# Kernel tuning notes

Hardware: AMD Instinct MI355X
Metric: run time of the kernel (lower is better)

The kernel has to match this reference:

```python
import jax, jax.numpy as jnp
import numpy as np


def setup_inputs() -> dict:
    key = jax.random.key(0)
    ks = jax.random.split(key, 8)
    B, S, T, H, A = 4, 1024, 256, 512, 256
    return {
        "encoder_outputs": jax.random.normal(ks[0], (B, S, H), dtype=jnp.float32),
        "decoder_hidden": jax.random.normal(ks[1], (B, T, H), dtype=jnp.float32),
        "Wh": jax.random.normal(ks[2], (H, A), dtype=jnp.float32) * (1.0 / np.sqrt(H)),
        "bh": jax.random.normal(ks[3], (A,), dtype=jnp.float32) * 0.01,
        "Ws": jax.random.normal(ks[4], (H, A), dtype=jnp.float32) * (1.0 / np.sqrt(H)),
        "bs": jax.random.normal(ks[5], (A,), dtype=jnp.float32) * 0.01,
        "Wv": jax.random.normal(ks[6], (A, 1), dtype=jnp.float32) * (1.0 / np.sqrt(A)),
        "bv": jax.random.normal(ks[7], (1,), dtype=jnp.float32) * 0.01,
    }


def reference(encoder_outputs, decoder_hidden, Wh, bh, Ws, bs, Wv, bv):
    # encoder_outputs: [B, S, H], decoder_hidden: [B, T, H]
    eh = encoder_outputs @ Wh + bh          # [B, S, A]
    dh = decoder_hidden @ Ws + bs           # [B, T, A]
    # broadcast-add (torch's unsqueeze+repeat is just a broadcast), tanh, then v-projection
    energy = jnp.tanh(eh[:, None, :, :] + dh[:, :, None, :])  # [B, T, S, A]
    scores = jnp.einsum("btsa,a->bts", energy, Wv[:, 0]) + bv[0]  # [B, T, S]
    return jax.nn.softmax(scores, axis=2)
```

## Files before the change

### kernel.cpp

```cpp
#include <hip/hip_runtime.h>

#define B_ 4
#define S_ 1024
#define T_ 256
#define H_ 512
#define A_ 256

typedef __attribute__((ext_vector_type(8))) short short8;
typedef __attribute__((ext_vector_type(4))) float f32x4;
typedef __attribute__((ext_vector_type(2))) float f32x2;

__device__ __forceinline__ float ex2(float x)   { return __builtin_amdgcn_exp2f(x); }
__device__ __forceinline__ float rcpf_(float x) { return __builtin_amdgcn_rcpf(x); }
__device__ __forceinline__ f32x2 splat2(float v) { f32x2 r; r.x = v; r.y = v; return r; }

#define K2F 2.8853900817779268f

__device__ __forceinline__ void split_bf16(float x, unsigned short& h, unsigned short& l)
{
    unsigned u = __float_as_uint(x);
    unsigned r = (u + 0x7FFFu + ((u >> 16) & 1u)) >> 16;
    h = (unsigned short)r;
    float hf = __uint_as_float(r << 16);
    float lo = x - hf;
    unsigned u2 = __float_as_uint(lo);
    l = (unsigned short)((u2 + 0x7FFFu + ((u2 >> 16) & 1u)) >> 16);
}

__global__ __launch_bounds__(256)
void prep_w(const float* __restrict__ Wh, const float* __restrict__ Wsm,
            unsigned short* __restrict__ WhTh, unsigned short* __restrict__ WhTl,
            unsigned short* __restrict__ WsTh, unsigned short* __restrict__ WsTl)
{
    __shared__ float lds[32][36];
    const int tid = threadIdx.x, bid = blockIdx.x;
    const int mat = bid >> 7, rem = bid & 127;
    const int k0 = (rem & 15) * 32, a0 = (rem >> 4) * 32;
    const float* W = mat ? Wsm : Wh;
    unsigned short* Oh = mat ? WsTh : WhTh;
    unsigned short* Ol = mat ? WsTl : WhTl;

    {
        int kl = tid >> 3, a4 = (tid & 7) * 4;
        float4 v = *(const float4*)&W[(size_t)(k0 + kl) * A_ + a0 + a4];
        lds[kl][a4] = v.x; lds[kl][a4 + 1] = v.y; lds[kl][a4 + 2] = v.z; lds[kl][a4 + 3] = v.w;
    }
    __syncthreads();
    {
        int al = tid >> 3, k4 = (tid & 7) * 4;
        unsigned short h[4], l[4];
        #pragma unroll
        for (int i = 0; i < 4; ++i) split_bf16(lds[k4 + i][al], h[i], l[i]);
        size_t o = (size_t)(a0 + al) * H_ + k0 + k4;
        *(ushort4*)&Oh[o] = make_ushort4(h[0], h[1], h[2], h[3]);
        *(ushort4*)&Ol[o] = make_ushort4(l[0], l[1], l[2], l[3]);
    }
}

__global__ __launch_bounds__(256)
void gemm_mfma(const float* __restrict__ enc, const float* __restrict__ dec,
               const unsigned short* __restrict__ WhTh, const unsigned short* __restrict__ WhTl,
               const unsigned short* __restrict__ WsTh, const unsigned short* __restrict__ WsTl,
               const float* __restrict__ bh, const float* __restrict__ bs,
               float* __restrict__ Ebuf, float* __restrict__ Dbuf)
{
    __shared__ short smem[8192];
    short* Ah = smem;
    short* Al = smem + 2048;
    short* Bh = smem + 4096;
    short* Bl = smem + 6144;

    const int tid = threadIdx.x, bid = blockIdx.x;
    const bool isE = bid < 256;
    int mb, nb;
    const float* Ag; const unsigned short* WTh; const unsigned short* WTl; const float* bias;
    if (isE) { mb = (bid & 63) * 64; nb = (bid >> 6) * 64; Ag = enc; WTh = WhTh; WTl = WhTl; bias = bh; }
    else { int b2 = bid - 256; mb = (b2 & 15) * 64; nb = (b2 >> 4) * 64; Ag = dec; WTh = WsTh; WTl = WsTl; bias = bs; }

    const int m_l = tid >> 2, q = tid & 3;
    const size_t arow = (size_t)(mb + m_l) * H_ + 8 * q;
    const size_t brow = (size_t)(nb + m_l) * H_ + 8 * q;
    const int woff = ((m_l >> 4) * 64 + (m_l & 15) + 16 * q) * 8;

    const int wave = tid >> 6, lane = tid & 63;
    const int wm = wave >> 1, wn = wave & 1;
    const int roffA = (2 * wm) * 512 + lane * 8;
    const int roffB = (2 * wn) * 512 + lane * 8;

    const int cl = lane & 15, rg = lane >> 4;
    const float bias0 = bias[nb + wn * 32 + cl];
    const float bias1 = bias[nb + wn * 32 + 16 + cl];

    f32x4 acc[2][2] = {};

    float4 aA = *(const float4*)&Ag[arow];
    float4 aB = *(const float4*)&Ag[arow + 4];
    short8 bHv = *(const short8*)&WTh[brow];
    short8 bLv = *(const short8*)&WTl[brow];

    for (int it = 0; it < 16; ++it) {
        __syncthreads();
        {
            float xs[8] = {aA.x, aA.y, aA.z, aA.w, aB.x, aB.y, aB.z, aB.w};
            short8 hv, lv;
            #pragma unroll
            for (int j = 0; j < 8; ++j) {
                unsigned short h, l; split_bf16(xs[j], h, l);
                hv[j] = (short)h; lv[j] = (short)l;
            }
            *(short8*)&Ah[woff] = hv;
            *(short8*)&Al[woff] = lv;
            *(short8*)&Bh[woff] = bHv;
            *(short8*)&Bl[woff] = bLv;
        }
        if (it < 15) {
            int kn = (it + 1) * 32;
            aA  = *(const float4*)&Ag[arow + kn];
            aB  = *(const float4*)&Ag[arow + kn + 4];
            bHv = *(const short8*)&WTh[brow + kn];
            bLv = *(const short8*)&WTl[brow + kn];
        }
        __syncthreads();
        short8 fAh0 = *(short8*)&Ah[roffA], fAh1 = *(short8*)&Ah[roffA + 512];
        short8 fAl0 = *(short8*)&Al[roffA], fAl1 = *(short8*)&Al[roffA + 512];
        short8 fBh0 = *(short8*)&Bh[roffB], fBh1 = *(short8*)&Bh[roffB + 512];
        short8 fBl0 = *(short8*)&Bl[roffB], fBl1 = *(short8*)&Bl[roffB + 512];
        acc[0][0] = __builtin_amdgcn_mfma_f32_16x16x32_bf16(fAh0, fBh0, acc[0][0], 0, 0, 0);
        acc[0][0] = __builtin_amdgcn_mfma_f32_16x16x32_bf16(fAh0, fBl0, acc[0][0], 0, 0, 0);
        acc[0][0] = __builtin_amdgcn_mfma_f32_16x16x32_bf16(fAl0, fBh0, acc[0][0], 0, 0, 0);
        acc[0][1] = __builtin_amdgcn_mfma_f32_16x16x32_bf16(fAh0, fBh1, acc[0][1], 0, 0, 0);
        acc[0][1] = __builtin_amdgcn_mfma_f32_16x16x32_bf16(fAh0, fBl1, acc[0][1], 0, 0, 0);
        acc[0][1] = __builtin_amdgcn_mfma_f32_16x16x32_bf16(fAl0, fBh1, acc[0][1], 0, 0, 0);
        acc[1][0] = __builtin_amdgcn_mfma_f32_16x16x32_bf16(fAh1, fBh0, acc[1][0], 0, 0, 0);
        acc[1][0] = __builtin_amdgcn_mfma_f32_16x16x32_bf16(fAh1, fBl0, acc[1][0], 0, 0, 0);
        acc[1][0] = __builtin_amdgcn_mfma_f32_16x16x32_bf16(fAl1, fBh0, acc[1][0], 0, 0, 0);
        acc[1][1] = __builtin_amdgcn_mfma_f32_16x16x32_bf16(fAh1, fBh1, acc[1][1], 0, 0, 0);
        acc[1][1] = __builtin_amdgcn_mfma_f32_16x16x32_bf16(fAh1, fBl1, acc[1][1], 0, 0, 0);
        acc[1][1] = __builtin_amdgcn_mfma_f32_16x16x32_bf16(fAl1, fBh1, acc[1][1], 0, 0, 0);
    }

    #pragma unroll
    for (int mf = 0; mf < 2; ++mf) {
        const int mg = mb + wm * 32 + mf * 16 + rg * 4;
        #pragma unroll
        for (int nf = 0; nf < 2; ++nf) {
            const int a = nb + wn * 32 + nf * 16 + cl;
            const float bb = nf ? bias1 : bias0;
            f32x4 ac = acc[mf][nf];
            float4 st;
            st.x = ex2((ac[0] + bb) * K2F);
            st.y = ex2((ac[1] + bb) * K2F);
            st.z = ex2((ac[2] + bb) * K2F);
            st.w = ex2((ac[3] + bb) * K2F);
            if (isE) {
                const int b = mg >> 10, s = mg & 1023;
                *(float4*)&Ebuf[(((size_t)b * A_ + a) << 10) + s] = st;
            } else {
                Dbuf[(size_t)(mg + 0) * A_ + a] = st.x;
                Dbuf[(size_t)(mg + 1) * A_ + a] = st.y;
                Dbuf[(size_t)(mg + 2) * A_ + a] = st.z;
                Dbuf[(size_t)(mg + 3) * A_ + a] = st.w;
            }
        }
    }
}

__device__ __forceinline__ void four_acc(const f32x2* ev, f32x2 d01, f32x2 d23,
                                         f32x2 w01, f32x2 w23, f32x2& acc)
{
    const f32x2 one = {1.0f, 1.0f};
    f32x2 q0 = __builtin_elementwise_fma(ev[0], splat2(d01.x), one);
    f32x2 q1 = __builtin_elementwise_fma(ev[1], splat2(d01.y), one);
    f32x2 q2 = __builtin_elementwise_fma(ev[2], splat2(d23.x), one);
    f32x2 q3 = __builtin_elementwise_fma(ev[3], splat2(d23.y), one);
    f32x2 q01 = q0 * q1, q23 = q2 * q3;
    f32x2 t01 = __builtin_elementwise_fma(splat2(w01.x), q1, splat2(w01.y) * q0);
    f32x2 t23 = __builtin_elementwise_fma(splat2(w23.x), q3, splat2(w23.y) * q2);
    f32x2 num = __builtin_elementwise_fma(t01, q23, t23 * q01);
    f32x2 den = q01 * q23;
    f32x2 r; r.x = rcpf_(den.x); r.y = rcpf_(den.y);
    acc = __builtin_elementwise_fma(num, r, acc);
}

#define LOADG(EV, DT, WW, G)                                            \
    { int ab_ = 4 * (G);                                                \
      EV[0] = *(const f32x2*)&Eb[(size_t)(ab_ + 0) << 10];              \
      EV[1] = *(const f32x2*)&Eb[(size_t)(ab_ + 1) << 10];              \
      EV[2] = *(const f32x2*)&Eb[(size_t)(ab_ + 2) << 10];              \
      EV[3] = *(const f32x2*)&Eb[(size_t)(ab_ + 3) << 10];              \
      DT[0] = *(const f32x2*)&Dsh[0][ab_];                              \
      DT[1] = *(const f32x2*)&Dsh[0][ab_ + 2];                          \
      DT[2] = *(const f32x2*)&Dsh[1][ab_];                              \
      DT[3] = *(const f32x2*)&Dsh[1][ab_ + 2];                          \
      WW[0] = *(const f32x2*)&Wsh[ab_];                                 \
      WW[1] = *(const f32x2*)&Wsh[ab_ + 2]; }

__global__ __launch_bounds__(512, 6)
void score_partial(const float* __restrict__ E, const float* __restrict__ D,
                   const float* __restrict__ Wv,
                   float* __restrict__ P0, float* __restrict__ P1)
{
    const int tid = threadIdx.x;
    const int bid = blockIdx.x;
    const int b   = bid >> 8;
    const int rem = bid & 255;
    const int h   = rem & 1;
    const int t0  = (rem >> 1) * 2;
    const int abase = h * 128;

    __shared__ float Dsh[2][128];
    __shared__ float Wsh[128];

    if (tid < 64) {
        int r = tid >> 5, c4 = (tid & 31) << 2;
        *(float4*)&Dsh[r][c4] = *(const float4*)&D[((size_t)b * T_ + t0 + r) * A_ + abase + c4];
    } else if (tid < 96) {
        int c4 = (tid - 64) << 2;
        *(float4*)&Wsh[c4] = *(const float4*)&Wv[abase + c4];
    }
    __syncthreads();

    const int s0 = tid << 1;
    const float* Eb = E + ((size_t)b * A_ + abase) * S_ + s0;

    f32x2 acc0 = {0.0f, 0.0f}, acc1 = {0.0f, 0.0f};
    f32x2 evA[4], evB[4], dA[4], dB[4], wA[2], wB[2];

    LOADG(evA, dA, wA, 0);
    for (int g = 0; g < 32; g += 2) {
        LOADG(evB, dB, wB, g + 1);
        four_acc(evA, dA[0], dA[1], wA[0], wA[1], acc0);
        four_acc(evA, dA[2], dA[3], wA[0], wA[1], acc1);
        if (g + 2 < 32) LOADG(evA, dA, wA, g + 2);
        four_acc(evB, dB[0], dB[1], wB[0], wB[1], acc0);
        four_acc(evB, dB[2], dB[3], wB[0], wB[1], acc1);
    }

    float* Pd = h ? P1 : P0;
    *(f32x2*)&Pd[((size_t)b * T_ + t0)     * S_ + s0] = acc0;
    *(f32x2*)&Pd[((size_t)b * T_ + t0 + 1) * S_ + s0] = acc1;
}
#undef LOADG

__global__ __launch_bounds__(256)
void merge_softmax(const float* __restrict__ P1, float* __restrict__ outp)
{
    const int row = blockIdx.x;
    const int tid = threadIdx.x;
    const int lane = tid & 63, wid = tid >> 6;
    __shared__ float red[4];

    float* o = outp + (size_t)row * S_;
    const float* p1 = P1 + (size_t)row * S_;
    const int s4 = tid << 2;

    float4 a = *(const float4*)&o[s4];
    float4 c = *(const float4*)&p1[s4];
    float e0 = ex2((a.x + c.x) * -K2F);
    float e1 = ex2((a.y + c.y) * -K2F);
    float e2 = ex2((a.z + c.z) * -K2F);
    float e3 = ex2((a.w + c.w) * -K2F);

    float ssum = (e0 + e1) + (e2 + e3);
    #pragma unroll
    for (int off = 32; off > 0; off >>= 1) ssum += __shfl_xor(ssum, off, 64);
    if (lane == 0) red[wid] = ssum;
    __syncthreads();
    float tot = (red[0] + red[1]) + (red[2] + red[3]);
    float inv = 1.0f / tot;

    *(float4*)&o[s4] = make_float4(e0 * inv, e1 * inv, e2 * inv, e3 * inv);
}

extern "C" void kernel_launch(void* const* d_in, const int* in_sizes, int n_in,
                              void* d_out, int out_size, void* d_ws, size_t ws_size,
                              hipStream_t stream)
{
    const float* enc = (const float*)d_in[0];
    const float* dec = (const float*)d_in[1];
    const float* Wh  = (const float*)d_in[2];
    const float* bh  = (const float*)d_in[3];
    const float* Wsm = (const float*)d_in[4];
    const float* bs  = (const float*)d_in[5];
    const float* Wv  = (const float*)d_in[6];

    float* Ebuf = (float*)d_ws;
    float* Dbuf = Ebuf + (size_t)B_ * A_ * S_;
    unsigned short* wt = (unsigned short*)(Dbuf + (size_t)B_ * T_ * A_);
    unsigned short* WhTh = wt;
    unsigned short* WhTl = wt + 131072;
    unsigned short* WsTh = wt + 262144;
    unsigned short* WsTl = wt + 393216;
    float* P1 = (float*)(wt + 524288);
    float* P0 = (float*)d_out;

    prep_w<<<256, 256, 0, stream>>>(Wh, Wsm, WhTh, WhTl, WsTh, WsTl);
    gemm_mfma<<<320, 256, 0, stream>>>(enc, dec, WhTh, WhTl, WsTh, WsTl,
                                       bh, bs, Ebuf, Dbuf);
    score_partial<<<B_ * 256, 512, 0, stream>>>(Ebuf, Dbuf, Wv, P0, P1);
    merge_softmax<<<B_ * T_, 256, 0, stream>>>(P1, (float*)d_out);
}
```

Measured before the change: 65.57 us.

## Retile score kernel to four decoder rows per block with A split four ways

The score kernel now processes four decoder time steps per block instead of two, so each loaded E vector is reused across more t rows. The A dimension is split into four partial slices instead of two when the workspace is large enough, which keeps the block count the same. The merge kernel now sums up to four partial buffers. This raises register pressure because the occupancy hint was dropped, and adds extra partial-buffer traffic in the merge step.

Measured after the change: 56.09 us. 14.5% less time.

```diff
diff --git a/kernel.cpp b/kernel.cpp
--- a/kernel.cpp
+++ b/kernel.cpp
@@ -8,11 +8,9 @@
 
 typedef __attribute__((ext_vector_type(8))) short short8;
 typedef __attribute__((ext_vector_type(4))) float f32x4;
-typedef __attribute__((ext_vector_type(2))) float f32x2;
 
 __device__ __forceinline__ float ex2(float x)   { return __builtin_amdgcn_exp2f(x); }
 __device__ __forceinline__ float rcpf_(float x) { return __builtin_amdgcn_rcpf(x); }
-__device__ __forceinline__ f32x2 splat2(float v) { f32x2 r; r.x = v; r.y = v; return r; }
 
 #define K2F 2.8853900817779268f
 
@@ -165,57 +163,32 @@
     }
 }
 
-__device__ __forceinline__ void four_acc(const f32x2* ev, f32x2 d01, f32x2 d23,
-                                         f32x2 w01, f32x2 w23, f32x2& acc)
-{
-    const f32x2 one = {1.0f, 1.0f};
-    f32x2 q0 = __builtin_elementwise_fma(ev[0], splat2(d01.x), one);
-    f32x2 q1 = __builtin_elementwise_fma(ev[1], splat2(d01.y), one);
-    f32x2 q2 = __builtin_elementwise_fma(ev[2], splat2(d23.x), one);
-    f32x2 q3 = __builtin_elementwise_fma(ev[3], splat2(d23.y), one);
-    f32x2 q01 = q0 * q1, q23 = q2 * q3;
-    f32x2 t01 = __builtin_elementwise_fma(splat2(w01.x), q1, splat2(w01.y) * q0);
-    f32x2 t23 = __builtin_elementwise_fma(splat2(w23.x), q3, splat2(w23.y) * q2);
-    f32x2 num = __builtin_elementwise_fma(t01, q23, t23 * q01);
-    f32x2 den = q01 * q23;
-    f32x2 r; r.x = rcpf_(den.x); r.y = rcpf_(den.y);
-    acc = __builtin_elementwise_fma(num, r, acc);
-}
-
-#define LOADG(EV, DT, WW, G)                                            \
-    { int ab_ = 4 * (G);                                                \
-      EV[0] = *(const f32x2*)&Eb[(size_t)(ab_ + 0) << 10];              \
-      EV[1] = *(const f32x2*)&Eb[(size_t)(ab_ + 1) << 10];              \
-      EV[2] = *(const f32x2*)&Eb[(size_t)(ab_ + 2) << 10];              \
-      EV[3] = *(const f32x2*)&Eb[(size_t)(ab_ + 3) << 10];              \
-      DT[0] = *(const f32x2*)&Dsh[0][ab_];                              \
-      DT[1] = *(const f32x2*)&Dsh[0][ab_ + 2];                          \
-      DT[2] = *(const f32x2*)&Dsh[1][ab_];                              \
-      DT[3] = *(const f32x2*)&Dsh[1][ab_ + 2];                          \
-      WW[0] = *(const f32x2*)&Wsh[ab_];                                 \
-      WW[1] = *(const f32x2*)&Wsh[ab_ + 2]; }
-
-__global__ __launch_bounds__(512, 6)
+template<int AS>
+__global__ __launch_bounds__(512)
 void score_partial(const float* __restrict__ E, const float* __restrict__ D,
                    const float* __restrict__ Wv,
-                   float* __restrict__ P0, float* __restrict__ P1)
-{
+                   float* __restrict__ P0, float* __restrict__ P1,
+                   float* __restrict__ P2, float* __restrict__ P3)
+{
+    constexpr int ABLK = 256 / AS;
+    constexpr int NG   = ABLK / 4;
+
     const int tid = threadIdx.x;
     const int bid = blockIdx.x;
-    const int b   = bid >> 8;
-    const int rem = bid & 255;
-    const int h   = rem & 1;
-    const int t0  = (rem >> 1) * 2;
-    const int abase = h * 128;
-
-    __shared__ float Dsh[2][128];
-    __shared__ float Wsh[128];
-
-    if (tid < 64) {
-        int r = tid >> 5, c4 = (tid & 31) << 2;
+    const int b   = bid / (64 * AS);
+    const int rem = bid % (64 * AS);
+    const int h   = rem & (AS - 1);
+    const int t0  = (rem / AS) * 4;
+    const int abase = h * ABLK;
+
+    __shared__ float Dsh[4][ABLK];
+    __shared__ float Wsh[ABLK];
+
+    if (tid < ABLK) {
+        int r = tid / (ABLK / 4), c4 = (tid % (ABLK / 4)) << 2;
         *(float4*)&Dsh[r][c4] = *(const float4*)&D[((size_t)b * T_ + t0 + r) * A_ + abase + c4];
-    } else if (tid < 96) {
-        int c4 = (tid - 64) << 2;
+    } else if (tid < ABLK + ABLK / 4) {
+        int c4 = (tid - ABLK) << 2;
         *(float4*)&Wsh[c4] = *(const float4*)&Wv[abase + c4];
     }
     __syncthreads();
@@ -223,27 +196,65 @@
     const int s0 = tid << 1;
     const float* Eb = E + ((size_t)b * A_ + abase) * S_ + s0;
 
-    f32x2 acc0 = {0.0f, 0.0f}, acc1 = {0.0f, 0.0f};
-    f32x2 evA[4], evB[4], dA[4], dB[4], wA[2], wB[2];
-
-    LOADG(evA, dA, wA, 0);
-    for (int g = 0; g < 32; g += 2) {
-        LOADG(evB, dB, wB, g + 1);
-        four_acc(evA, dA[0], dA[1], wA[0], wA[1], acc0);
-        four_acc(evA, dA[2], dA[3], wA[0], wA[1], acc1);
-        if (g + 2 < 32) LOADG(evA, dA, wA, g + 2);
-        four_acc(evB, dB[0], dB[1], wB[0], wB[1], acc0);
-        four_acc(evB, dB[2], dB[3], wB[0], wB[1], acc1);
-    }
-
-    float* Pd = h ? P1 : P0;
-    *(f32x2*)&Pd[((size_t)b * T_ + t0)     * S_ + s0] = acc0;
-    *(f32x2*)&Pd[((size_t)b * T_ + t0 + 1) * S_ + s0] = acc1;
-}
-#undef LOADG
-
+    float accx[4] = {}, accy[4] = {};
+    float2 evA[4], evB[4];
+
+    #pragma unroll
+    for (int j = 0; j < 4; ++j) evA[j] = *(const float2*)&Eb[(size_t)j * S_];
+
+    auto compute = [&](const float2* ev, int g) {
+        float4 w = *(const float4*)&Wsh[g * 4];
+        #pragma unroll
+        for (int t = 0; t < 4; ++t) {
+            float4 d = *(const float4*)&Dsh[t][g * 4];
+            {
+                float q0 = fmaf(ev[0].x, d.x, 1.0f);
+                float q1 = fmaf(ev[1].x, d.y, 1.0f);
+                float q2 = fmaf(ev[2].x, d.z, 1.0f);
+                float q3 = fmaf(ev[3].x, d.w, 1.0f);
+                float q01 = q0 * q1, q23 = q2 * q3;
+                float n1 = fmaf(w.x, q1, w.y * q0);
+                float n2 = fmaf(w.z, q3, w.w * q2);
+                float num = fmaf(n1, q23, n2 * q01);
+                accx[t] = fmaf(num, rcpf_(q01 * q23), accx[t]);
+            }
+            {
+                float q0 = fmaf(ev[0].y, d.x, 1.0f);
+                float q1 = fmaf(ev[1].y, d.y, 1.0f);
+                float q2 = fmaf(ev[2].y, d.z, 1.0f);
+                float q3 = fmaf(ev[3].y, d.w, 1.0f);
+                float q01 = q0 * q1, q23 = q2 * q3;
+                float n1 = fmaf(w.x, q1, w.y * q0);
+                float n2 = fmaf(w.z, q3, w.w * q2);
+                float num = fmaf(n1, q23, n2 * q01);
+                accy[t] = fmaf(num, rcpf_(q01 * q23), accy[t]);
+            }
+        }
+    };
+
+    for (int g = 0; g < NG; g += 2) {
+        #pragma unroll
+        for (int j = 0; j < 4; ++j) evB[j] = *(const float2*)&Eb[(size_t)((g + 1) * 4 + j) * S_];
+        compute(evA, g);
+        if (g + 2 < NG) {
+            #pragma unroll
+            for (int j = 0; j < 4; ++j) evA[j] = *(const float2*)&Eb[(size_t)((g + 2) * 4 + j) * S_];
+        }
+        compute(evB, g + 1);
+    }
+
+    float* Pd = (h == 0) ? P0 : (h == 1) ? P1 : (h == 2) ? P2 : P3;
+    #pragma unroll
+    for (int t = 0; t < 4; ++t) {
+        float2 o; o.x = accx[t]; o.y = accy[t];
+        *(float2*)&Pd[((size_t)b * T_ + t0 + t) * S_ + s0] = o;
+    }
+}
+
+template<int NP>
 __global__ __launch_bounds__(256)
-void merge_softmax(const float* __restrict__ P1, float* __restrict__ outp)
+void merge_softmax(const float* __restrict__ P1, const float* __restrict__ P2,
+                   const float* __restrict__ P3, float* __restrict__ outp)
 {
     const int row = blockIdx.x;
     const int tid = threadIdx.x;
@@ -251,15 +262,23 @@
     __shared__ float red[4];
 
     float* o = outp + (size_t)row * S_;
-    const float* p1 = P1 + (size_t)row * S_;
     const int s4 = tid << 2;
 
     float4 a = *(const float4*)&o[s4];
-    float4 c = *(const float4*)&p1[s4];
-    float e0 = ex2((a.x + c.x) * -K2F);
-    float e1 = ex2((a.y + c.y) * -K2F);
-    float e2 = ex2((a.z + c.z) * -K2F);
-    float e3 = ex2((a.w + c.w) * -K2F);
+    {
+        float4 c = *(const float4*)&P1[(size_t)row * S_ + s4];
+        a.x += c.x; a.y += c.y; a.z += c.z; a.w += c.w;
+    }
+    if (NP >= 4) {
+        float4 c = *(const float4*)&P2[(size_t)row * S_ + s4];
+        a.x += c.x; a.y += c.y; a.z += c.z; a.w += c.w;
+        float4 e = *(const float4*)&P3[(size_t)row * S_ + s4];
+        a.x += e.x; a.y += e.y; a.z += e.z; a.w += e.w;
+    }
+    float e0 = ex2(a.x * -K2F);
+    float e1 = ex2(a.y * -K2F);
+    float e2 = ex2(a.z * -K2F);
+    float e3 = ex2(a.w * -K2F);
 
     float ssum = (e0 + e1) + (e2 + e3);
     #pragma unroll
@@ -284,19 +303,27 @@
     const float* bs  = (const float*)d_in[5];
     const float* Wv  = (const float*)d_in[6];
 
-    float* Ebuf = (float*)d_ws;
-    float* Dbuf = Ebuf + (size_t)B_ * A_ * S_;
-    unsigned short* wt = (unsigned short*)(Dbuf + (size_t)B_ * T_ * A_);
+    char* ws = (char*)d_ws;
+    float* Ebuf = (float*)ws;
+    float* Dbuf = (float*)(ws + (4 << 20));
+    unsigned short* wt = (unsigned short*)(ws + (5 << 20));
     unsigned short* WhTh = wt;
     unsigned short* WhTl = wt + 131072;
     unsigned short* WsTh = wt + 262144;
     unsigned short* WsTl = wt + 393216;
-    float* P1 = (float*)(wt + 524288);
+    float* P1 = (float*)(ws + (6 << 20));
+    float* P2 = (float*)(ws + (10 << 20));
+    float* P3 = (float*)(ws + (14 << 20));
     float* P0 = (float*)d_out;
 
     prep_w<<<256, 256, 0, stream>>>(Wh, Wsm, WhTh, WhTl, WsTh, WsTl);
     gemm_mfma<<<320, 256, 0, stream>>>(enc, dec, WhTh, WhTl, WsTh, WsTl,
                                        bh, bs, Ebuf, Dbuf);
-    score_partial<<<B_ * 256, 512, 0, stream>>>(Ebuf, Dbuf, Wv, P0, P1);
-    merge_softmax<<<B_ * T_, 256, 0, stream>>>(P1, (float*)d_out);
-}
+    if (ws_size >= (size_t)(18 << 20)) {
+        score_partial<4><<<B_ * 256, 512, 0, stream>>>(Ebuf, Dbuf, Wv, P0, P1, P2, P3);
+        merge_softmax<4><<<B_ * T_, 256, 0, stream>>>(P1, P2, P3, (float*)d_out);
+    } else {
+        score_partial<2><<<B_ * 128, 512, 0, stream>>>(Ebuf, Dbuf, Wv, P0, P1, P2, P3);
+        merge_softmax<2><<<B_ * T_, 256, 0, stream>>>(P1, P2, P3, (float*)d_out);
+    }
+}
```
